# Optimization experiments

Hardware: AMD Instinct MI355X
Metric: run time of the kernel (lower is better)

Reference implementation:

```python
import jax, jax.numpy as jnp
import numpy as np

N_LEVELS = 16
F_PER_LEVEL = 2
LOG2_T = 19
TABLE_SIZE = 1 << LOG2_T
BASE_RES = 16.0
FINEST_RES = 512.0
# W == H == 512 -> x1 = y1 = 1.0
BOX_MIN = jnp.array([-1.0, -1.0], dtype=jnp.float32)
BOX_MAX = jnp.array([1.0, 1.0], dtype=jnp.float32)
# corner offsets, same order as torch BOX_OFFSETS: (0,0),(0,1),(1,0),(1,1)
OFFSETS = jnp.array([[i, j] for i in (0, 1) for j in (0, 1)], dtype=jnp.int32)
PRIME0 = jnp.uint32(1)
PRIME1 = jnp.uint32(2654435761)
HASH_MASK = jnp.uint32(TABLE_SIZE - 1)


def setup_inputs() -> dict:
    key = jax.random.key(0)
    ks = jax.random.split(key, 8)
    B, P = 4, 262144
    coord_2D = jax.random.uniform(ks[0], (B, P, 2), dtype=jnp.float32)  # in [0,1) subset of box
    embeddings = jax.random.normal(ks[1], (N_LEVELS, TABLE_SIZE, F_PER_LEVEL), dtype=jnp.float32)
    d_in = 2 + N_LEVELS * F_PER_LEVEL  # 34
    W0 = jax.random.normal(ks[2], (d_in, 256), dtype=jnp.float32) * 0.05
    b0 = jnp.zeros((256,), dtype=jnp.float32)
    W1 = jax.random.normal(ks[3], (256, 256), dtype=jnp.float32) * 0.05
    b1 = jnp.zeros((256,), dtype=jnp.float32)
    W2 = jax.random.normal(ks[4], (256, 3), dtype=jnp.float32) * 0.05
    b2 = jnp.zeros((3,), dtype=jnp.float32)
    return {"coord_2D": coord_2D, "embeddings": embeddings,
            "W0": W0, "b0": b0, "W1": W1, "b1": b1, "W2": W2, "b2": b2}


def _hash(corners_int32):
    # corners: [N,4,2] int32; xor of per-dim prime products, masked to table size (uint32 wraparound semantics)
    c = corners_int32.astype(jnp.uint32)
    h = (c[..., 0] * PRIME0) ^ (c[..., 1] * PRIME1)
    return (h & HASH_MASK).astype(jnp.int32)


def _encode(xy, embeddings):
    # xy: [N,2]; embeddings: [L, T, F]
    b = np.exp((np.log(FINEST_RES) - np.log(BASE_RES)) / (N_LEVELS - 1))
    resolutions = jnp.floor(BASE_RES * (b ** jnp.arange(N_LEVELS, dtype=jnp.float32)))  # [L]

    def level_encode(table, res):
        grid = (BOX_MAX - BOX_MIN) / res                     # [2]
        bl = jnp.floor((xy - BOX_MIN) / grid).astype(jnp.int32)  # bottom-left cell idx [N,2]
        vmin = bl.astype(xy.dtype) * grid + BOX_MIN          # voxel min vertex [N,2]
        w = (xy - vmin) / grid                               # bilinear weights [N,2]
        corners = bl[:, None, :] + OFFSETS                   # [N,4,2]
        emb = table[_hash(corners)]                          # gather: [N,4,F]
        wx = w[:, 0:1]
        wy = w[:, 1:2]
        c00 = emb[:, 0] * (1 - wx) + emb[:, 2] * wx
        c01 = emb[:, 1] * (1 - wx) + emb[:, 3] * wx
        return c00 * (1 - wy) + c01 * wy                     # [N,F]

    enc = jax.vmap(level_encode)(embeddings, resolutions)    # [L,N,F]
    return jnp.moveaxis(enc, 0, 1).reshape(xy.shape[0], N_LEVELS * F_PER_LEVEL)


def reference(coord_2D, embeddings, W0, b0, W1, b1, W2, b2):
    B = coord_2D.shape[0]
    xy = jnp.clip(coord_2D.reshape(-1, 2), BOX_MIN, BOX_MAX)
    enc = _encode(xy, embeddings)
    points_enc = jnp.concatenate([xy, enc], axis=-1)         # [N, 34]
    feat = jax.nn.relu(points_enc @ W0 + b0)
    feat = jax.nn.relu(feat @ W1 + b1)
    rgb = jax.nn.sigmoid(feat @ W2 + b2)
    return rgb.reshape(B, -1, 3)
```

## Files before the change

kernel.cpp:

```cpp
#include <hip/hip_runtime.h>
#include <hip/hip_bf16.h>
#include <cstdint>
#include <cstddef>

#define N_LEVELS   16
#define LOG2_T     19
#define TABLE_SIZE (1u << LOG2_T)
#define HASH_MASK  (TABLE_SIZE - 1u)
#define PRIME1     2654435761u

#define TPB 256
#define BT  64

typedef __attribute__((ext_vector_type(8))) short short8;
typedef __attribute__((ext_vector_type(4))) float floatx4;

__device__ __constant__ float c_res[N_LEVELS] = {
    16.f, 20.f, 25.f, 32.f, 40.f, 50.f, 64.f, 80.f,
    101.f, 128.f, 161.f, 203.f, 256.f, 322.f, 406.f, 512.f
};

__device__ __forceinline__ unsigned short f2bf(float x) {
    union { float f; uint32_t u; } v; v.f = x;
    const uint32_t u = v.u;
    return (unsigned short)((u + 0x7fffu + ((u >> 16) & 1u)) >> 16);
}

__device__ __forceinline__ uint32_t pk_bf16(float a, float b) {
#if __has_builtin(__builtin_amdgcn_cvt_pk_bf16_f32)
    typedef __attribute__((ext_vector_type(2))) __bf16 bf16x2;
    bf16x2 v = __builtin_amdgcn_cvt_pk_bf16_f32(a, b);
    uint32_t u; __builtin_memcpy(&u, &v, 4); return u;
#else
    return (uint32_t)f2bf(a) | ((uint32_t)f2bf(b) << 16);
#endif
}

__device__ __forceinline__ int fswz(int row, int cb) {
    return (row << 7) + (cb ^ ((row & 7) << 4));
}
__device__ __forceinline__ int hswz(int row, int cb) {
    return (row << 9) + (cb ^ ((row & 7) << 4));
}

__global__ void pack_weights(const float* __restrict__ W0,
                             const float* __restrict__ W1,
                             const float* __restrict__ W2,
                             unsigned short* __restrict__ ws)
{
    const int f = blockIdx.x;
    const int lane = threadIdx.x;
    const int q = lane >> 4, r = lane & 15;
    int layer, kt, nt;
    if (f < 32)       { layer = 0; kt = f >> 4;        nt = f & 15; }
    else if (f < 160) { layer = 1; kt = (f - 32) >> 4; nt = (f - 32) & 15; }
    else              { layer = 2; kt = f - 160;       nt = 0; }
    unsigned short vals[8];
    #pragma unroll
    for (int j = 0; j < 8; ++j) {
        const int k = kt * 32 + q * 8 + j;
        const int n = nt * 16 + r;
        float v = 0.f;
        if (layer == 0) {
            if (k < 32)       v = W0[(2 + k) * 256 + n];
            else if (k == 32) v = W0[0 * 256 + n];
            else if (k == 33) v = W0[1 * 256 + n];
        } else if (layer == 1) {
            v = W1[k * 256 + n];
        } else {
            if (n < 3) v = W2[k * 3 + n];
        }
        vals[j] = f2bf(v);
    }
    uint4 pk;
    pk.x = (uint32_t)vals[0] | ((uint32_t)vals[1] << 16);
    pk.y = (uint32_t)vals[2] | ((uint32_t)vals[3] << 16);
    pk.z = (uint32_t)vals[4] | ((uint32_t)vals[5] << 16);
    pk.w = (uint32_t)vals[6] | ((uint32_t)vals[7] << 16);
    *(uint4*)(ws + (size_t)f * 1024 + lane * 8) = pk;
}

__global__ __launch_bounds__(TPB, 4)
void fused_ngp_mlp(const float* __restrict__ coord,
                   const float* __restrict__ emb,
                   const unsigned short* __restrict__ wpack,
                   const float* __restrict__ b0,
                   const float* __restrict__ b1,
                   const float* __restrict__ b2,
                   float* __restrict__ out, int npoints)
{
    __shared__ __attribute__((aligned(16))) unsigned char feat[BT * 128];
    __shared__ __attribute__((aligned(16))) unsigned char h[BT * 512];

    const int t = threadIdx.x;
    const int p0 = blockIdx.x * BT;
    const int wave = t >> 6;
    const int lane = t & 63;
    const int q = lane >> 4, r = lane & 15;

    {
        const int p = t >> 2;
        const int k = t & 3;
        const int gp = p0 + p;
        float x = 0.f, y = 0.f;
        if (gp < npoints) {
            x = coord[2 * gp + 0]; y = coord[2 * gp + 1];
            x = fminf(fmaxf(x, -1.f), 1.f);
            y = fminf(fmaxf(y, -1.f), 1.f);
        }
        if (k == 0) {
            uint4 z; z.x = pk_bf16(x, y); z.y = 0u; z.z = 0u; z.w = 0u;
            *(uint4*)(feat + fswz(p, 64)) = z;
        } else {
            const uint4 z = {0u, 0u, 0u, 0u};
            *(uint4*)(feat + fswz(p, 64 + 16 * k)) = z;
        }
        #pragma unroll
        for (int i = 0; i < 4; ++i) {
            const int l = 4 * k + i;
            const float res  = c_res[l];
            const float grid = 2.0f / res;
            const float invg = res * 0.5f;
            const float tx = (x + 1.0f) / grid;
            const float ty = (y + 1.0f) / grid;
            const int bx = (int)floorf(tx);
            const int by = (int)floorf(ty);
            const float vx = (float)bx * grid - 1.0f;
            const float vy = (float)by * grid - 1.0f;
            const float wx = (x - vx) * invg;
            const float wy = (y - vy) * invg;
            const float2* tab = (const float2*)emb + (size_t)l * TABLE_SIZE;
            const uint32_t ux0 = (uint32_t)bx, ux1 = (uint32_t)(bx + 1);
            const uint32_t hy0 = (uint32_t)by * PRIME1;
            const uint32_t hy1 = (uint32_t)(by + 1) * PRIME1;
            const float2 e00 = tab[(ux0 ^ hy0) & HASH_MASK];
            const float2 e01 = tab[(ux0 ^ hy1) & HASH_MASK];
            const float2 e10 = tab[(ux1 ^ hy0) & HASH_MASK];
            const float2 e11 = tab[(ux1 ^ hy1) & HASH_MASK];
            const float owx = 1.f - wx, owy = 1.f - wy;
            const float f0 = (e00.x * owx + e10.x * wx) * owy + (e01.x * owx + e11.x * wx) * wy;
            const float f1 = (e00.y * owx + e10.y * wx) * owy + (e01.y * owx + e11.y * wx) * wy;
            *(uint32_t*)(feat + fswz(p, 16 * k + 4 * i)) = pk_bf16(f0, f1);
        }
    }
    __syncthreads();

    const unsigned short* w0p = wpack;
    const unsigned short* w1p = wpack + 32 * 1024;
    const unsigned short* w2p = wpack + 160 * 1024;

    {
        floatx4 acc[4][4];
        #pragma unroll
        for (int mti = 0; mti < 4; ++mti)
            #pragma unroll
            for (int nt = 0; nt < 4; ++nt)
                acc[mti][nt] = floatx4{0.f, 0.f, 0.f, 0.f};
        #pragma unroll
        for (int kt = 0; kt < 2; ++kt) {
            short8 a[4], b[4];
            #pragma unroll
            for (int mti = 0; mti < 4; ++mti)
                a[mti] = *(const short8*)(w0p + (size_t)(kt * 16 + wave * 4 + mti) * 1024 + lane * 8);
            #pragma unroll
            for (int nt = 0; nt < 4; ++nt)
                b[nt] = *(const short8*)(feat + fswz(16 * nt + r, 64 * kt + 16 * q));
            #pragma unroll
            for (int mti = 0; mti < 4; ++mti)
                #pragma unroll
                for (int nt = 0; nt < 4; ++nt)
                    acc[mti][nt] = __builtin_amdgcn_mfma_f32_16x16x32_bf16(a[mti], b[nt], acc[mti][nt], 0, 0, 0);
        }
        #pragma unroll
        for (int mti = 0; mti < 4; ++mti) {
            const int col = (wave * 4 + mti) * 16 + 4 * q;
            const float4 bias = *(const float4*)&b0[col];
            #pragma unroll
            for (int nt = 0; nt < 4; ++nt) {
                const floatx4 a = acc[mti][nt];
                uint2 v;
                v.x = pk_bf16(fmaxf(a[0] + bias.x, 0.f), fmaxf(a[1] + bias.y, 0.f));
                v.y = pk_bf16(fmaxf(a[2] + bias.z, 0.f), fmaxf(a[3] + bias.w, 0.f));
                *(uint2*)(h + hswz(16 * nt + r, 2 * col)) = v;
            }
        }
    }
    __syncthreads();

    {
        floatx4 acc[4][4];
        #pragma unroll
        for (int mti = 0; mti < 4; ++mti)
            #pragma unroll
            for (int nt = 0; nt < 4; ++nt)
                acc[mti][nt] = floatx4{0.f, 0.f, 0.f, 0.f};
        #pragma unroll 2
        for (int kt = 0; kt < 8; ++kt) {
            short8 a[4], b[4];
            #pragma unroll
            for (int mti = 0; mti < 4; ++mti)
                a[mti] = *(const short8*)(w1p + (size_t)(kt * 16 + wave * 4 + mti) * 1024 + lane * 8);
            #pragma unroll
            for (int nt = 0; nt < 4; ++nt)
                b[nt] = *(const short8*)(h + hswz(16 * nt + r, 64 * kt + 16 * q));
            #pragma unroll
            for (int mti = 0; mti < 4; ++mti)
                #pragma unroll
                for (int nt = 0; nt < 4; ++nt)
                    acc[mti][nt] = __builtin_amdgcn_mfma_f32_16x16x32_bf16(a[mti], b[nt], acc[mti][nt], 0, 0, 0);
        }
        __syncthreads();
        #pragma unroll
        for (int mti = 0; mti < 4; ++mti) {
            const int col = (wave * 4 + mti) * 16 + 4 * q;
            const float4 bias = *(const float4*)&b1[col];
            #pragma unroll
            for (int nt = 0; nt < 4; ++nt) {
                const floatx4 a = acc[mti][nt];
                uint2 v;
                v.x = pk_bf16(fmaxf(a[0] + bias.x, 0.f), fmaxf(a[1] + bias.y, 0.f));
                v.y = pk_bf16(fmaxf(a[2] + bias.z, 0.f), fmaxf(a[3] + bias.w, 0.f));
                *(uint2*)(h + hswz(16 * nt + r, 2 * col)) = v;
            }
        }
    }
    __syncthreads();

    {
        floatx4 acc = floatx4{0.f, 0.f, 0.f, 0.f};
        #pragma unroll
        for (int kt = 0; kt < 8; ++kt) {
            const short8 a = *(const short8*)(w2p + (size_t)kt * 1024 + lane * 8);
            const short8 b = *(const short8*)(h + hswz(16 * wave + r, 64 * kt + 16 * q));
            acc = __builtin_amdgcn_mfma_f32_16x16x32_bf16(a, b, acc, 0, 0, 0);
        }
        if (q == 0) {
            const int gp = p0 + 16 * wave + r;
            if (gp < npoints) {
                #pragma unroll
                for (int reg = 0; reg < 3; ++reg) {
                    const float s = acc[reg] + b2[reg];
                    out[(size_t)gp * 3 + reg] = 1.f / (1.f + expf(-s));
                }
            }
        }
    }
}

extern "C" void kernel_launch(void* const* d_in, const int* in_sizes, int n_in,
                              void* d_out, int out_size, void* d_ws, size_t ws_size,
                              hipStream_t stream) {
    const float* coord = (const float*)d_in[0];
    const float* emb   = (const float*)d_in[1];
    const float* W0    = (const float*)d_in[2];
    const float* b0    = (const float*)d_in[3];
    const float* W1    = (const float*)d_in[4];
    const float* b1    = (const float*)d_in[5];
    const float* W2    = (const float*)d_in[6];
    const float* b2    = (const float*)d_in[7];
    float* out = (float*)d_out;
    unsigned short* ws = (unsigned short*)d_ws;

    const int npoints = in_sizes[0] / 2;
    const int blocks  = (npoints + BT - 1) / BT;

    hipLaunchKernelGGL(pack_weights, dim3(168), dim3(64), 0, stream, W0, W1, W2, ws);
    hipLaunchKernelGGL(fused_ngp_mlp, dim3(blocks), dim3(TPB), 0, stream,
                       coord, emb, ws, b0, b1, b2, out, npoints);
}
```

Baseline: 358.1 us.

## Double block tile to 128 points, reassign gather per wave, nontemporal loads on fine levels

Block size grows to 512 threads handling 128 points, and each wave now gathers one group of 4 levels for 64 points, writing a single 16-byte vector to LDS. The MLP tiling changes to 2 M-tiles by 8 N-tiles per wave, so each weight fragment is reused across more points and fewer global weight loads are issued per point. The finer levels (groups 2-3) use nontemporal loads so their scattered accesses are meant to pollute cache less for the coarse levels. The bigger tile doubles LDS per block, and with launch_bounds still set to 4 blocks of 512 threads, register limits may tighten and occupancy may drop. The final layer and output code, which are not shown, may also depend on the old wave and point layout.

```diff
diff --git a/kernel.cpp b/kernel.cpp
--- a/kernel.cpp
+++ b/kernel.cpp
@@ -9,11 +9,12 @@
 #define HASH_MASK  (TABLE_SIZE - 1u)
 #define PRIME1     2654435761u
 
-#define TPB 256
-#define BT  64
+#define TPB 512
+#define BT  128
 
 typedef __attribute__((ext_vector_type(8))) short short8;
 typedef __attribute__((ext_vector_type(4))) float floatx4;
+typedef __attribute__((ext_vector_type(2))) float f32x2;
 
 __device__ __constant__ float c_res[N_LEVELS] = {
     16.f, 20.f, 25.f, 32.f, 40.f, 50.f, 64.f, 80.f,
@@ -80,6 +81,48 @@
     *(uint4*)(ws + (size_t)f * 1024 + lane * 8) = pk;
 }
 
+template<bool NT>
+__device__ __forceinline__ void enc_gather(int g, float x, float y,
+                                           const f32x2* __restrict__ emb2,
+                                           float (&wxa)[4], float (&wya)[4],
+                                           f32x2 (&e)[4][4])
+{
+    #pragma unroll
+    for (int i = 0; i < 4; ++i) {
+        const int l = 4 * g + i;
+        const float res  = c_res[l];
+        const float grid = 2.0f / res;
+        const float invg = res * 0.5f;
+        const float tx = (x + 1.0f) / grid;
+        const float ty = (y + 1.0f) / grid;
+        const int bx = (int)floorf(tx);
+        const int by = (int)floorf(ty);
+        const float vx = (float)bx * grid - 1.0f;
+        const float vy = (float)by * grid - 1.0f;
+        wxa[i] = (x - vx) * invg;
+        wya[i] = (y - vy) * invg;
+        const f32x2* tab = emb2 + (size_t)l * TABLE_SIZE;
+        const uint32_t ux0 = (uint32_t)bx, ux1 = (uint32_t)(bx + 1);
+        const uint32_t hy0 = (uint32_t)by * PRIME1;
+        const uint32_t hy1 = (uint32_t)(by + 1) * PRIME1;
+        const uint32_t i00 = (ux0 ^ hy0) & HASH_MASK;
+        const uint32_t i01 = (ux0 ^ hy1) & HASH_MASK;
+        const uint32_t i10 = (ux1 ^ hy0) & HASH_MASK;
+        const uint32_t i11 = (ux1 ^ hy1) & HASH_MASK;
+        if (NT) {
+            e[i][0] = __builtin_nontemporal_load(tab + i00);
+            e[i][1] = __builtin_nontemporal_load(tab + i01);
+            e[i][2] = __builtin_nontemporal_load(tab + i10);
+            e[i][3] = __builtin_nontemporal_load(tab + i11);
+        } else {
+            e[i][0] = tab[i00];
+            e[i][1] = tab[i01];
+            e[i][2] = tab[i10];
+            e[i][3] = tab[i11];
+        }
+    }
+}
+
 __global__ __launch_bounds__(TPB, 4)
 void fused_ngp_mlp(const float* __restrict__ coord,
                    const float* __restrict__ emb,
@@ -100,7 +143,7 @@
 
     {
         const int p = t >> 2;
-        const int k = t & 3;
+        const int sg = t & 3;
         const int gp = p0 + p;
         float x = 0.f, y = 0.f;
         if (gp < npoints) {
@@ -108,40 +151,39 @@
             x = fminf(fmaxf(x, -1.f), 1.f);
             y = fminf(fmaxf(y, -1.f), 1.f);
         }
-        if (k == 0) {
-            uint4 z; z.x = pk_bf16(x, y); z.y = 0u; z.z = 0u; z.w = 0u;
-            *(uint4*)(feat + fswz(p, 64)) = z;
-        } else {
-            const uint4 z = {0u, 0u, 0u, 0u};
-            *(uint4*)(feat + fswz(p, 64 + 16 * k)) = z;
-        }
+        uint4 z = {0u, 0u, 0u, 0u};
+        if (sg == 0) z.x = pk_bf16(x, y);
+        *(uint4*)(feat + fswz(p, 64 + 16 * sg)) = z;
+    }
+
+    {
+        const int g = wave & 3;
+        const int p = ((wave >> 2) << 6) + lane;
+        const int gp = p0 + p;
+        float x = 0.f, y = 0.f;
+        if (gp < npoints) {
+            x = coord[2 * gp + 0]; y = coord[2 * gp + 1];
+            x = fminf(fmaxf(x, -1.f), 1.f);
+            y = fminf(fmaxf(y, -1.f), 1.f);
+        }
+        float wxa[4], wya[4];
+        f32x2 e[4][4];
+        const f32x2* emb2 = (const f32x2*)emb;
+        if (g >= 2) enc_gather<true >(g, x, y, emb2, wxa, wya, e);
+        else        enc_gather<false>(g, x, y, emb2, wxa, wya, e);
+        uint32_t vv[4];
         #pragma unroll
         for (int i = 0; i < 4; ++i) {
-            const int l = 4 * k + i;
-            const float res  = c_res[l];
-            const float grid = 2.0f / res;
-            const float invg = res * 0.5f;
-            const float tx = (x + 1.0f) / grid;
-            const float ty = (y + 1.0f) / grid;
-            const int bx = (int)floorf(tx);
-            const int by = (int)floorf(ty);
-            const float vx = (float)bx * grid - 1.0f;
-            const float vy = (float)by * grid - 1.0f;
-            const float wx = (x - vx) * invg;
-            const float wy = (y - vy) * invg;
-            const float2* tab = (const float2*)emb + (size_t)l * TABLE_SIZE;
-            const uint32_t ux0 = (uint32_t)bx, ux1 = (uint32_t)(bx + 1);
-            const uint32_t hy0 = (uint32_t)by * PRIME1;
-            const uint32_t hy1 = (uint32_t)(by + 1) * PRIME1;
-            const float2 e00 = tab[(ux0 ^ hy0) & HASH_MASK];
-            const float2 e01 = tab[(ux0 ^ hy1) & HASH_MASK];
-            const float2 e10 = tab[(ux1 ^ hy0) & HASH_MASK];
-            const float2 e11 = tab[(ux1 ^ hy1) & HASH_MASK];
+            const float wx = wxa[i], wy = wya[i];
             const float owx = 1.f - wx, owy = 1.f - wy;
-            const float f0 = (e00.x * owx + e10.x * wx) * owy + (e01.x * owx + e11.x * wx) * wy;
-            const float f1 = (e00.y * owx + e10.y * wx) * owy + (e01.y * owx + e11.y * wx) * wy;
-            *(uint32_t*)(feat + fswz(p, 16 * k + 4 * i)) = pk_bf16(f0, f1);
-        }
+            const float f0 = (e[i][0].x * owx + e[i][2].x * wx) * owy
+                           + (e[i][1].x * owx + e[i][3].x * wx) * wy;
+            const float f1 = (e[i][0].y * owx + e[i][2].y * wx) * owy
+                           + (e[i][1].y * owx + e[i][3].y * wx) * wy;
+            vv[i] = pk_bf16(f0, f1);
+        }
+        uint4 v; v.x = vv[0]; v.y = vv[1]; v.z = vv[2]; v.w = vv[3];
+        *(uint4*)(feat + fswz(p, 16 * g)) = v;
     }
     __syncthreads();
 
@@ -150,33 +192,32 @@
     const unsigned short* w2p = wpack + 160 * 1024;
 
     {
-        floatx4 acc[4][4];
-        #pragma unroll
-        for (int mti = 0; mti < 4; ++mti)
-            #pragma unroll
-            for (int nt = 0; nt < 4; ++nt)
+        floatx4 acc[2][8];
+        #pragma unroll
+        for (int mti = 0; mti < 2; ++mti)
+            #pragma unroll
+            for (int nt = 0; nt < 8; ++nt)
                 acc[mti][nt] = floatx4{0.f, 0.f, 0.f, 0.f};
         #pragma unroll
         for (int kt = 0; kt < 2; ++kt) {
-            short8 a[4], b[4];
-            #pragma unroll
-            for (int mti = 0; mti < 4; ++mti)
-                a[mti] = *(const short8*)(w0p + (size_t)(kt * 16 + wave * 4 + mti) * 1024 + lane * 8);
-            #pragma unroll
-            for (int nt = 0; nt < 4; ++nt)
-                b[nt] = *(const short8*)(feat + fswz(16 * nt + r, 64 * kt + 16 * q));
-            #pragma unroll
-            for (int mti = 0; mti < 4; ++mti)
+            short8 a[2];
+            #pragma unroll
+            for (int mti = 0; mti < 2; ++mti)
+                a[mti] = *(const short8*)(w0p + (size_t)(kt * 16 + wave * 2 + mti) * 1024 + lane * 8);
+            #pragma unroll
+            for (int nt = 0; nt < 8; ++nt) {
+                const short8 b = *(const short8*)(feat + fswz(16 * nt + r, 64 * kt + 16 * q));
                 #pragma unroll
-                for (int nt = 0; nt < 4; ++nt)
-                    acc[mti][nt] = __builtin_amdgcn_mfma_f32_16x16x32_bf16(a[mti], b[nt], acc[mti][nt], 0, 0, 0);
-        }
-        #pragma unroll
-        for (int mti = 0; mti < 4; ++mti) {
-            const int col = (wave * 4 + mti) * 16 + 4 * q;
+                for (int mti = 0; mti < 2; ++mti)
+                    acc[mti][nt] = __builtin_amdgcn_mfma_f32_16x16x32_bf16(a[mti], b, acc[mti][nt], 0, 0, 0);
+            }
+        }
+        #pragma unroll
+        for (int mti = 0; mti < 2; ++mti) {
+            const int col = (wave * 2 + mti) * 16 + 4 * q;
             const float4 bias = *(const float4*)&b0[col];
             #pragma unroll
-            for (int nt = 0; nt < 4; ++nt) {
+            for (int nt = 0; nt < 8; ++nt) {
                 const floatx4 a = acc[mti][nt];
                 uint2 v;
                 v.x = pk_bf16(fmaxf(a[0] + bias.x, 0.f), fmaxf(a[1] + bias.y, 0.f));
@@ -188,34 +229,33 @@
     __syncthreads();
 
     {
-        floatx4 acc[4][4];
-        #pragma unroll
-        for (int mti = 0; mti < 4; ++mti)
-            #pragma unroll
-            for (int nt = 0; nt < 4; ++nt)
+        floatx4 acc[2][8];
+        #pragma unroll
+        for (int mti = 0; mti < 2; ++mti)
+            #pragma unroll
+            for (int nt = 0; nt < 8; ++nt)
                 acc[mti][nt] = floatx4{0.f, 0.f, 0.f, 0.f};
         #pragma unroll 2
         for (int kt = 0; kt < 8; ++kt) {
-            short8 a[4], b[4];
-            #pragma unroll
-            for (int mti = 0; mti < 4; ++mti)
-                a[mti] = *(const short8*)(w1p + (size_t)(kt * 16 + wave * 4 + mti) * 1024 + lane * 8);
-            #pragma unroll
-            for (int nt = 0; nt < 4; ++nt)
-                b[nt] = *(const short8*)(h + hswz(16 * nt + r, 64 * kt + 16 * q));
-            #pragma unroll
-            for (int mti = 0; mti < 4; ++mti)
+            short8 a[2];
+            #pragma unroll
+            for (int mti = 0; mti < 2; ++mti)
+                a[mti] = *(const short8*)(w1p + (size_t)(kt * 16 + wave * 2 + mti) * 1024 + lane * 8);
+            #pragma unroll
+            for (int nt = 0; nt < 8; ++nt) {
+                const short8 b = *(const short8*)(h + hswz(16 * nt + r, 64 * kt + 16 * q));
                 #pragma unroll
-                for (int nt = 0; nt < 4; ++nt)
-                    acc[mti][nt] = __builtin_amdgcn_mfma_f32_16x16x32_bf16(a[mti], b[nt], acc[mti][nt], 0, 0, 0);
+                for (int mti = 0; mti < 2; ++mti)
+                    acc[mti][nt] = __builtin_amdgcn_mfma_f32_16x16x32_bf16(a[mti], b, acc[mti][nt], 0, 0, 0);
+            }
         }
         __syncthreads();
         #pragma unroll
-        for (int mti = 0; mti < 4; ++mti) {
-            const int col = (wave * 4 + mti) * 16 + 4 * q;
+        for (int mti = 0; mti < 2; ++mti) {
+            const int col = (wave * 2 + mti) * 16 + 4 * q;
             const float4 bias = *(const float4*)&b1[col];
             #pragma unroll
-            for (int nt = 0; nt < 4; ++nt) {
+            for (int nt = 0; nt < 8; ++nt) {
                 const floatx4 a = acc[mti][nt];
                 uint2 v;
                 v.x = pk_bf16(fmaxf(a[0] + bias.x, 0.f), fmaxf(a[1] + bias.y, 0.f));
```

After: 362.1 us. Within noise of the previous version (+1.1%).

## Spatially sort points by 512x512 grid bin before hash-grid encoding

Applied to the files above, without the earlier changes.

Adds a counting sort (histogram, two-level scan, atomic scatter) that reorders points by a 512x512 spatial bin, so neighbouring points in a block hit the same hash-table entries and gathers get better cache locality. The fused kernel reads the sorted coordinates and writes results back through the permutation. It also remaps workgroup order across 8 groups (likely for XCD locality) and restructures the encode so each wave handles 4 levels for 64 points with all gathers issued before the interpolation. The price is five extra launches, atomics on a 1 MB histogram and a scattered output write.

```diff
diff --git a/kernel.cpp b/kernel.cpp
--- a/kernel.cpp
+++ b/kernel.cpp
@@ -12,8 +12,12 @@
 #define TPB 256
 #define BT  64
 
+#define SORT_RES 512
+#define NBINS    (SORT_RES * SORT_RES)
+
 typedef __attribute__((ext_vector_type(8))) short short8;
 typedef __attribute__((ext_vector_type(4))) float floatx4;
+typedef __attribute__((ext_vector_type(2))) float f32x2;
 
 __device__ __constant__ float c_res[N_LEVELS] = {
     16.f, 20.f, 25.f, 32.f, 40.f, 50.f, 64.f, 80.f,
@@ -41,6 +45,83 @@
 }
 __device__ __forceinline__ int hswz(int row, int cb) {
     return (row << 9) + (cb ^ ((row & 7) << 4));
+}
+
+__device__ __forceinline__ int bin_of(float2 c) {
+    const float x = fminf(fmaxf(c.x, -1.f), 1.f);
+    const float y = fminf(fmaxf(c.y, -1.f), 1.f);
+    const int bx = (int)fminf((x + 1.0f) * 256.0f, 511.0f);
+    const int by = (int)fminf((y + 1.0f) * 256.0f, 511.0f);
+    return by * SORT_RES + bx;
+}
+
+__global__ void k_zero(uint32_t* __restrict__ p) {
+    const int i = blockIdx.x * blockDim.x + threadIdx.x;
+    uint4 z = {0u, 0u, 0u, 0u};
+    *(uint4*)(p + i * 4) = z;
+}
+
+__global__ void k_hist(const float2* __restrict__ xy, uint32_t* __restrict__ hist, int n) {
+    const int i = blockIdx.x * blockDim.x + threadIdx.x;
+    if (i >= n) return;
+    atomicAdd(hist + bin_of(xy[i]), 1u);
+}
+
+__global__ void k_scan1(uint32_t* __restrict__ hist, uint32_t* __restrict__ sums) {
+    __shared__ uint32_t lds[256];
+    const int t = threadIdx.x;
+    const int base = blockIdx.x * 1024 + t * 4;
+    uint4 v = *(uint4*)(hist + base);
+    const uint32_t s = v.x + v.y + v.z + v.w;
+    lds[t] = s;
+    __syncthreads();
+    #pragma unroll
+    for (int off = 1; off < 256; off <<= 1) {
+        const uint32_t val = lds[t];
+        const uint32_t add = (t >= off) ? lds[t - off] : 0u;
+        __syncthreads();
+        lds[t] = val + add;
+        __syncthreads();
+    }
+    const uint32_t incl = lds[t];
+    const uint32_t excl = incl - s;
+    uint4 o;
+    o.x = excl;
+    o.y = excl + v.x;
+    o.z = excl + v.x + v.y;
+    o.w = excl + v.x + v.y + v.z;
+    *(uint4*)(hist + base) = o;
+    if (t == 255) sums[blockIdx.x] = incl;
+}
+
+__global__ void k_scan2(uint32_t* __restrict__ sums) {
+    __shared__ uint32_t lds[256];
+    const int t = threadIdx.x;
+    const uint32_t s = sums[t];
+    lds[t] = s;
+    __syncthreads();
+    #pragma unroll
+    for (int off = 1; off < 256; off <<= 1) {
+        const uint32_t val = lds[t];
+        const uint32_t add = (t >= off) ? lds[t - off] : 0u;
+        __syncthreads();
+        lds[t] = val + add;
+        __syncthreads();
+    }
+    sums[t] = lds[t] - s;
+}
+
+__global__ void k_scatter(const float2* __restrict__ xy, uint32_t* __restrict__ hist,
+                          const uint32_t* __restrict__ sums, int* __restrict__ perm,
+                          float2* __restrict__ sxy, int n) {
+    const int i = blockIdx.x * blockDim.x + threadIdx.x;
+    if (i >= n) return;
+    const float2 c = xy[i];
+    const int b = bin_of(c);
+    const uint32_t loc = atomicAdd(hist + b, 1u);
+    const uint32_t pos = sums[b >> 10] + loc;
+    perm[pos] = i;
+    sxy[pos] = c;
 }
 
 __global__ void pack_weights(const float* __restrict__ W0,
@@ -81,7 +162,8 @@
 }
 
 __global__ __launch_bounds__(TPB, 4)
-void fused_ngp_mlp(const float* __restrict__ coord,
+void fused_ngp_mlp(const float2* __restrict__ xy,
+                   const int* __restrict__ perm,
                    const float* __restrict__ emb,
                    const unsigned short* __restrict__ wpack,
                    const float* __restrict__ b0,
@@ -93,31 +175,45 @@
     __shared__ __attribute__((aligned(16))) unsigned char h[BT * 512];
 
     const int t = threadIdx.x;
-    const int p0 = blockIdx.x * BT;
+    int wg = blockIdx.x;
+    const int nwg = gridDim.x;
+    if ((nwg & 7) == 0) wg = (wg & 7) * (nwg >> 3) + (wg >> 3);
+    const int p0 = wg * BT;
     const int wave = t >> 6;
     const int lane = t & 63;
     const int q = lane >> 4, r = lane & 15;
 
     {
         const int p = t >> 2;
-        const int k = t & 3;
+        const int sg = t & 3;
         const int gp = p0 + p;
         float x = 0.f, y = 0.f;
         if (gp < npoints) {
-            x = coord[2 * gp + 0]; y = coord[2 * gp + 1];
-            x = fminf(fmaxf(x, -1.f), 1.f);
-            y = fminf(fmaxf(y, -1.f), 1.f);
-        }
-        if (k == 0) {
-            uint4 z; z.x = pk_bf16(x, y); z.y = 0u; z.z = 0u; z.w = 0u;
-            *(uint4*)(feat + fswz(p, 64)) = z;
-        } else {
-            const uint4 z = {0u, 0u, 0u, 0u};
-            *(uint4*)(feat + fswz(p, 64 + 16 * k)) = z;
-        }
+            const float2 c = xy[gp];
+            x = fminf(fmaxf(c.x, -1.f), 1.f);
+            y = fminf(fmaxf(c.y, -1.f), 1.f);
+        }
+        uint4 z = {0u, 0u, 0u, 0u};
+        if (sg == 0) z.x = pk_bf16(x, y);
+        *(uint4*)(feat + fswz(p, 64 + 16 * sg)) = z;
+    }
+
+    {
+        const int g = wave;
+        const int p = lane;
+        const int gp = p0 + p;
+        float x = 0.f, y = 0.f;
+        if (gp < npoints) {
+            const float2 c = xy[gp];
+            x = fminf(fmaxf(c.x, -1.f), 1.f);
+            y = fminf(fmaxf(c.y, -1.f), 1.f);
+        }
+        float wxa[4], wya[4];
+        f32x2 e[4][4];
+        const f32x2* emb2 = (const f32x2*)emb;
         #pragma unroll
         for (int i = 0; i < 4; ++i) {
-            const int l = 4 * k + i;
+            const int l = 4 * g + i;
             const float res  = c_res[l];
             const float grid = 2.0f / res;
             const float invg = res * 0.5f;
@@ -127,21 +223,30 @@
             const int by = (int)floorf(ty);
             const float vx = (float)bx * grid - 1.0f;
             const float vy = (float)by * grid - 1.0f;
-            const float wx = (x - vx) * invg;
-            const float wy = (y - vy) * invg;
-            const float2* tab = (const float2*)emb + (size_t)l * TABLE_SIZE;
+            wxa[i] = (x - vx) * invg;
+            wya[i] = (y - vy) * invg;
+            const f32x2* tab = emb2 + (size_t)l * TABLE_SIZE;
             const uint32_t ux0 = (uint32_t)bx, ux1 = (uint32_t)(bx + 1);
             const uint32_t hy0 = (uint32_t)by * PRIME1;
             const uint32_t hy1 = (uint32_t)(by + 1) * PRIME1;
-            const float2 e00 = tab[(ux0 ^ hy0) & HASH_MASK];
-            const float2 e01 = tab[(ux0 ^ hy1) & HASH_MASK];
-            const float2 e10 = tab[(ux1 ^ hy0) & HASH_MASK];
-            const float2 e11 = tab[(ux1 ^ hy1) & HASH_MASK];
+            e[i][0] = tab[(ux0 ^ hy0) & HASH_MASK];
+            e[i][1] = tab[(ux0 ^ hy1) & HASH_MASK];
+            e[i][2] = tab[(ux1 ^ hy0) & HASH_MASK];
+            e[i][3] = tab[(ux1 ^ hy1) & HASH_MASK];
+        }
+        uint32_t vv[4];
+        #pragma unroll
+        for (int i = 0; i < 4; ++i) {
+            const float wx = wxa[i], wy = wya[i];
             const float owx = 1.f - wx, owy = 1.f - wy;
-            const float f0 = (e00.x * owx + e10.x * wx) * owy + (e01.x * owx + e11.x * wx) * wy;
-            const float f1 = (e00.y * owx + e10.y * wx) * owy + (e01.y * owx + e11.y * wx) * wy;
-            *(uint32_t*)(feat + fswz(p, 16 * k + 4 * i)) = pk_bf16(f0, f1);
-        }
+            const float f0 = (e[i][0].x * owx + e[i][2].x * wx) * owy
+                           + (e[i][1].x * owx + e[i][3].x * wx) * wy;
+            const float f1 = (e[i][0].y * owx + e[i][2].y * wx) * owy
+                           + (e[i][1].y * owx + e[i][3].y * wx) * wy;
+            vv[i] = pk_bf16(f0, f1);
+        }
+        uint4 v; v.x = vv[0]; v.y = vv[1]; v.z = vv[2]; v.w = vv[3];
+        *(uint4*)(feat + fswz(p, 16 * g)) = v;
     }
     __syncthreads();
 
@@ -237,10 +342,11 @@
         if (q == 0) {
             const int gp = p0 + 16 * wave + r;
             if (gp < npoints) {
+                const int oi = perm ? perm[gp] : gp;
                 #pragma unroll
                 for (int reg = 0; reg < 3; ++reg) {
                     const float s = acc[reg] + b2[reg];
-                    out[(size_t)gp * 3 + reg] = 1.f / (1.f + expf(-s));
+                    out[(size_t)oi * 3 + reg] = 1.f / (1.f + expf(-s));
                 }
             }
         }
@@ -259,12 +365,39 @@
     const float* W2    = (const float*)d_in[6];
     const float* b2    = (const float*)d_in[7];
     float* out = (float*)d_out;
-    unsigned short* ws = (unsigned short*)d_ws;
+    unsigned char* ws = (unsigned char*)d_ws;
 
     const int npoints = in_sizes[0] / 2;
     const int blocks  = (npoints + BT - 1) / BT;
 
-    hipLaunchKernelGGL(pack_weights, dim3(168), dim3(64), 0, stream, W0, W1, W2, ws);
-    hipLaunchKernelGGL(fused_ngp_mlp, dim3(blocks), dim3(TPB), 0, stream,
-                       coord, emb, ws, b0, b1, b2, out, npoints);
-}
+    const size_t W_BYTES   = 168 * 1024 * 2;
+    const size_t off_hist  = W_BYTES;
+    const size_t off_sums  = off_hist + (size_t)NBINS * 4;
+    const size_t off_perm  = off_sums + 1024;
+    size_t off_sxy = off_perm + (size_t)npoints * 4;
+    off_sxy = (off_sxy + 15) & ~(size_t)15;
+    const size_t required  = off_sxy + (size_t)npoints * 8;
+
+    unsigned short* wp = (unsigned short*)(ws);
+    hipLaunchKernelGGL(pack_weights, dim3(168), dim3(64), 0, stream, W0, W1, W2, wp);
+
+    if (ws_size >= required && npoints > 0) {
+        uint32_t* hist = (uint32_t*)(ws + off_hist);
+        uint32_t* sums = (uint32_t*)(ws + off_sums);
+        int*      perm = (int*)(ws + off_perm);
+        float2*   sxy  = (float2*)(ws + off_sxy);
+        const float2* cxy = (const float2*)coord;
+
+        const int pb = (npoints + 255) / 256;
+        hipLaunchKernelGGL(k_zero,    dim3(NBINS / 1024), dim3(256), 0, stream, hist);
+        hipLaunchKernelGGL(k_hist,    dim3(pb),  dim3(256), 0, stream, cxy, hist, npoints);
+        hipLaunchKernelGGL(k_scan1,   dim3(256), dim3(256), 0, stream, hist, sums);
+        hipLaunchKernelGGL(k_scan2,   dim3(1),   dim3(256), 0, stream, sums);
+        hipLaunchKernelGGL(k_scatter, dim3(pb),  dim3(256), 0, stream, cxy, hist, sums, perm, sxy, npoints);
+        hipLaunchKernelGGL(fused_ngp_mlp, dim3(blocks), dim3(TPB), 0, stream,
+                           sxy, perm, emb, wp, b0, b1, b2, out, npoints);
+    } else {
+        hipLaunchKernelGGL(fused_ngp_mlp, dim3(blocks), dim3(TPB), 0, stream,
+                           (const float2*)coord, (const int*)nullptr, emb, wp, b0, b1, b2, out, npoints);
+    }
+}
```

New measurement: 481.3 us. +34.4%, slower.

## Remap hash-grid encoding so each wave handles one level group per point

Applied to the files above, without the earlier changes.

The encoding stage is remapped so each wave processes four consecutive levels for 64 consecutive points, with lanes indexing points. Within a wave all lanes then gather from the same level table, and each lane writes one 16-byte feature chunk. The hidden-layer LDS swizzle gains an extra XOR term to reduce bank conflicts, bias+ReLU uses packed two-wide float ops, and the resolution table becomes a compile-time constant instead of constant memory. Coordinates are now loaded twice per thread, and the extra swizzle term must stay consistent between writes and reads.

```diff
diff --git a/kernel.cpp b/kernel.cpp
--- a/kernel.cpp
+++ b/kernel.cpp
@@ -14,11 +14,15 @@
 
 typedef __attribute__((ext_vector_type(8))) short short8;
 typedef __attribute__((ext_vector_type(4))) float floatx4;
-
-__device__ __constant__ float c_res[N_LEVELS] = {
-    16.f, 20.f, 25.f, 32.f, 40.f, 50.f, 64.f, 80.f,
-    101.f, 128.f, 161.f, 203.f, 256.f, 322.f, 406.f, 512.f
-};
+typedef __attribute__((ext_vector_type(2))) float f32x2;
+
+__device__ __forceinline__ constexpr float resf(int l) {
+    constexpr float r[N_LEVELS] = {
+        16.f, 20.f, 25.f, 32.f, 40.f, 50.f, 64.f, 80.f,
+        101.f, 128.f, 161.f, 203.f, 256.f, 322.f, 406.f, 512.f
+    };
+    return r[l];
+}
 
 __device__ __forceinline__ unsigned short f2bf(float x) {
     union { float f; uint32_t u; } v; v.f = x;
@@ -40,7 +44,8 @@
     return (row << 7) + (cb ^ ((row & 7) << 4));
 }
 __device__ __forceinline__ int hswz(int row, int cb) {
-    return (row << 9) + (cb ^ ((row & 7) << 4));
+    const int c = row & 7;
+    return (row << 9) + (cb ^ ((c << 4) ^ (c << 6)));
 }
 
 __global__ void pack_weights(const float* __restrict__ W0,
@@ -80,8 +85,59 @@
     *(uint4*)(ws + (size_t)f * 1024 + lane * 8) = pk;
 }
 
+template<int G>
+__device__ __forceinline__ uint4 encode4(float x, float y, const char* __restrict__ ebase)
+{
+    uint32_t vv[4];
+    #pragma unroll
+    for (int i = 0; i < 4; ++i) {
+        const int l = 4 * G + i;
+        const float res  = resf(l);
+        const float grid = 2.0f / res;
+        const float invg = res * 0.5f;
+        const float tx = (x + 1.0f) / grid;
+        const float ty = (y + 1.0f) / grid;
+        const int bx = (int)floorf(tx);
+        const int by = (int)floorf(ty);
+        const float wx = (x - ((float)bx * grid - 1.0f)) * invg;
+        const float wy = (y - ((float)by * grid - 1.0f)) * invg;
+        const uint32_t hy0 = (uint32_t)by * PRIME1;
+        const uint32_t hy1 = hy0 + PRIME1;
+        const uint32_t ux0 = (uint32_t)bx;
+        const uint32_t ux1 = ux0 + 1u;
+        const uint32_t lb = (uint32_t)l << (LOG2_T + 3);
+        const f32x2 e00 = *(const f32x2*)(ebase + (lb + (((ux0 ^ hy0) & HASH_MASK) << 3)));
+        const f32x2 e01 = *(const f32x2*)(ebase + (lb + (((ux0 ^ hy1) & HASH_MASK) << 3)));
+        const f32x2 e10 = *(const f32x2*)(ebase + (lb + (((ux1 ^ hy0) & HASH_MASK) << 3)));
+        const f32x2 e11 = *(const f32x2*)(ebase + (lb + (((ux1 ^ hy1) & HASH_MASK) << 3)));
+        const float owx = 1.f - wx, owy = 1.f - wy;
+        const float f0 = (e00.x * owx + e10.x * wx) * owy + (e01.x * owx + e11.x * wx) * wy;
+        const float f1 = (e00.y * owx + e10.y * wx) * owy + (e01.y * owx + e11.y * wx) * wy;
+        vv[i] = pk_bf16(f0, f1);
+    }
+    uint4 v; v.x = vv[0]; v.y = vv[1]; v.z = vv[2]; v.w = vv[3];
+    return v;
+}
+
+__device__ __forceinline__ uint2 bias_relu_pk(const floatx4 a, const float4 bias)
+{
+    const f32x2 z = {0.f, 0.f};
+    f32x2 v01 = {a[0], a[1]};
+    f32x2 v23 = {a[2], a[3]};
+    const f32x2 b01 = {bias.x, bias.y};
+    const f32x2 b23 = {bias.z, bias.w};
+    v01 += b01;
+    v23 += b23;
+    v01 = __builtin_elementwise_max(v01, z);
+    v23 = __builtin_elementwise_max(v23, z);
+    uint2 r;
+    r.x = pk_bf16(v01.x, v01.y);
+    r.y = pk_bf16(v23.x, v23.y);
+    return r;
+}
+
 __global__ __launch_bounds__(TPB, 4)
-void fused_ngp_mlp(const float* __restrict__ coord,
+void fused_ngp_mlp(const float2* __restrict__ xy,
                    const float* __restrict__ emb,
                    const unsigned short* __restrict__ wpack,
                    const float* __restrict__ b0,
@@ -100,48 +156,37 @@
 
     {
         const int p = t >> 2;
-        const int k = t & 3;
+        const int sg = t & 3;
         const int gp = p0 + p;
         float x = 0.f, y = 0.f;
         if (gp < npoints) {
-            x = coord[2 * gp + 0]; y = coord[2 * gp + 1];
-            x = fminf(fmaxf(x, -1.f), 1.f);
-            y = fminf(fmaxf(y, -1.f), 1.f);
-        }
-        if (k == 0) {
-            uint4 z; z.x = pk_bf16(x, y); z.y = 0u; z.z = 0u; z.w = 0u;
-            *(uint4*)(feat + fswz(p, 64)) = z;
-        } else {
-            const uint4 z = {0u, 0u, 0u, 0u};
-            *(uint4*)(feat + fswz(p, 64 + 16 * k)) = z;
-        }
-        #pragma unroll
-        for (int i = 0; i < 4; ++i) {
-            const int l = 4 * k + i;
-            const float res  = c_res[l];
-            const float grid = 2.0f / res;
-            const float invg = res * 0.5f;
-            const float tx = (x + 1.0f) / grid;
-            const float ty = (y + 1.0f) / grid;
-            const int bx = (int)floorf(tx);
-            const int by = (int)floorf(ty);
-            const float vx = (float)bx * grid - 1.0f;
-            const float vy = (float)by * grid - 1.0f;
-            const float wx = (x - vx) * invg;
-            const float wy = (y - vy) * invg;
-            const float2* tab = (const float2*)emb + (size_t)l * TABLE_SIZE;
-            const uint32_t ux0 = (uint32_t)bx, ux1 = (uint32_t)(bx + 1);
-            const uint32_t hy0 = (uint32_t)by * PRIME1;
-            const uint32_t hy1 = (uint32_t)(by + 1) * PRIME1;
-            const float2 e00 = tab[(ux0 ^ hy0) & HASH_MASK];
-            const float2 e01 = tab[(ux0 ^ hy1) & HASH_MASK];
-            const float2 e10 = tab[(ux1 ^ hy0) & HASH_MASK];
-            const float2 e11 = tab[(ux1 ^ hy1) & HASH_MASK];
-            const float owx = 1.f - wx, owy = 1.f - wy;
-            const float f0 = (e00.x * owx + e10.x * wx) * owy + (e01.x * owx + e11.x * wx) * wy;
-            const float f1 = (e00.y * owx + e10.y * wx) * owy + (e01.y * owx + e11.y * wx) * wy;
-            *(uint32_t*)(feat + fswz(p, 16 * k + 4 * i)) = pk_bf16(f0, f1);
-        }
+            const float2 c = xy[gp];
+            x = fminf(fmaxf(c.x, -1.f), 1.f);
+            y = fminf(fmaxf(c.y, -1.f), 1.f);
+        }
+        uint4 z = {0u, 0u, 0u, 0u};
+        if (sg == 0) z.x = pk_bf16(x, y);
+        *(uint4*)(feat + fswz(p, 64 + 16 * sg)) = z;
+    }
+
+    {
+        const int p = lane;
+        const int gp = p0 + p;
+        float x = 0.f, y = 0.f;
+        if (gp < npoints) {
+            const float2 c = xy[gp];
+            x = fminf(fmaxf(c.x, -1.f), 1.f);
+            y = fminf(fmaxf(c.y, -1.f), 1.f);
+        }
+        const char* ebase = (const char*)emb;
+        uint4 v;
+        switch (wave) {
+            case 0:  v = encode4<0>(x, y, ebase); break;
+            case 1:  v = encode4<1>(x, y, ebase); break;
+            case 2:  v = encode4<2>(x, y, ebase); break;
+            default: v = encode4<3>(x, y, ebase); break;
+        }
+        *(uint4*)(feat + fswz(p, 16 * wave)) = v;
     }
     __syncthreads();
 
@@ -177,10 +222,7 @@
             const float4 bias = *(const float4*)&b0[col];
             #pragma unroll
             for (int nt = 0; nt < 4; ++nt) {
-                const floatx4 a = acc[mti][nt];
-                uint2 v;
-                v.x = pk_bf16(fmaxf(a[0] + bias.x, 0.f), fmaxf(a[1] + bias.y, 0.f));
-                v.y = pk_bf16(fmaxf(a[2] + bias.z, 0.f), fmaxf(a[3] + bias.w, 0.f));
+                const uint2 v = bias_relu_pk(acc[mti][nt], bias);
                 *(uint2*)(h + hswz(16 * nt + r, 2 * col)) = v;
             }
         }
@@ -216,10 +258,7 @@
             const float4 bias = *(const float4*)&b1[col];
             #pragma unroll
             for (int nt = 0; nt < 4; ++nt) {
-                const floatx4 a = acc[mti][nt];
-                uint2 v;
-                v.x = pk_bf16(fmaxf(a[0] + bias.x, 0.f), fmaxf(a[1] + bias.y, 0.f));
-                v.y = pk_bf16(fmaxf(a[2] + bias.z, 0.f), fmaxf(a[3] + bias.w, 0.f));
+                const uint2 v = bias_relu_pk(acc[mti][nt], bias);
                 *(uint2*)(h + hswz(16 * nt + r, 2 * col)) = v;
             }
         }
@@ -266,5 +305,5 @@
 
     hipLaunchKernelGGL(pack_weights, dim3(168), dim3(64), 0, stream, W0, W1, W2, ws);
     hipLaunchKernelGGL(fused_ngp_mlp, dim3(blocks), dim3(TPB), 0, stream,
-                       coord, emb, ws, b0, b1, b2, out, npoints);
-}
+                       (const float2*)coord, emb, ws, b0, b1, b2, out, npoints);
+}
```

After: 355.1 us. No clear change (-0.8%).
